# Kernel optimization log

Hardware: AMD Instinct MI355X
Metric: run time of the kernel (lower is better)

Reference implementation:

```python
import jax, jax.numpy as jnp
import numpy as np

N, D, H, E, K = 16384, 1024, 4096, 8, 2
EPS = 1e-5


def setup_inputs() -> dict:
    key = jax.random.key(0)
    ks = jax.random.split(key, 12)
    s = 0.02
    return {
        "x": jax.random.normal(ks[0], (N, D), dtype=jnp.float32),
        "ln_g": jnp.ones((D,), jnp.float32),
        "ln_b": jnp.zeros((D,), jnp.float32),
        "r_w1": jax.random.normal(ks[1], (D, H // 2), jnp.float32) * s,
        "r_b1": jnp.zeros((H // 2,), jnp.float32),
        "r_w2": jax.random.normal(ks[2], (H // 2, E), jnp.float32) * s,
        "r_b2": jnp.zeros((E,), jnp.float32),
        "e_w1": jax.random.normal(ks[3], (E, D, H), jnp.float32) * s,
        "e_b1": jnp.zeros((E, H), jnp.float32),
        "e_w2": jax.random.normal(ks[4], (E, H, D), jnp.float32) * s,
        "e_b2": jnp.zeros((E, D), jnp.float32),
    }


def reference(x, ln_g, ln_b, r_w1, r_b1, r_w2, r_b2, e_w1, e_b1, e_w2, e_b2):
    # LayerNorm
    mu = jnp.mean(x, axis=-1, keepdims=True)
    var = jnp.mean(jnp.square(x - mu), axis=-1, keepdims=True)
    xn = (x - mu) * jax.lax.rsqrt(var + EPS) * ln_g + ln_b  # [N, D]

    # Router: Linear -> ReLU -> Linear -> softmax -> top-k, renormalize
    logits = jax.nn.relu(xn @ r_w1 + r_b1) @ r_w2 + r_b2  # [N, E]
    probs = jax.nn.softmax(logits, axis=-1)
    vals, idx = jax.lax.top_k(probs, K)  # [N, K]
    vals = vals / jnp.sum(vals, axis=-1, keepdims=True)

    # Dense expert dispatch: loop over fixed small E, weight by combine gate
    out = jnp.zeros_like(x)
    for e in range(E):
        gate = jnp.sum(vals * (idx == e).astype(vals.dtype), axis=-1)  # [N]
        h = jax.nn.relu(xn @ e_w1[e] + e_b1[e])  # dropout in eval mode -> identity
        y = h @ e_w2[e] + e_b2[e]  # [N, D]
        out = out + gate[:, None] * y
    return x + out
```

## Files before the change

kernel.cpp:

```cpp
#include <hip/hip_runtime.h>
#include <cstdint>
#include <cstddef>

typedef unsigned short u16;
typedef __attribute__((ext_vector_type(8))) short bf16x8;
typedef __attribute__((ext_vector_type(4))) float f32x4;

#define N_TOK 16384
#define DIM   1024
#define HID   4096
#define NEXP  8
#define HR    2048
#define TAU   0.02f
#define MAXMT 264
#define MAXMT2 136

__device__ __forceinline__ u16 f2bf(float f) {
  union { float f; uint32_t u; } x; x.f = f;
  uint32_t r = x.u + 0x7FFFu + ((x.u >> 16) & 1u);
  return (u16)(r >> 16);
}
__device__ __forceinline__ float bf2f(u16 u) {
  union { uint32_t u; float f; } x; x.u = ((uint32_t)u) << 16; return x.f;
}

__device__ __forceinline__ void async16(const void* g, const void* l) {
  auto gp = reinterpret_cast<const __attribute__((address_space(1))) uint32_t*>(
      reinterpret_cast<uintptr_t>(g));
  auto lp = reinterpret_cast<__attribute__((address_space(3))) uint32_t*>(
      reinterpret_cast<uintptr_t>(l));
  __builtin_amdgcn_global_load_lds(gp, lp, 16, 0, 0);
}

__device__ __forceinline__ unsigned xcd_swz(unsigned flat, unsigned nwg) {
  const unsigned xcd = flat & 7u, lid = flat >> 3;
  const unsigned q = nwg >> 3, r = nwg & 7u;
  return (xcd < r ? xcd * (q + 1u) : r * (q + 1u) + (xcd - r) * q) + lid;
}

template<bool SPLIT>
__global__ __launch_bounds__(256)
void transpose_cvt(const float* __restrict__ src, u16* __restrict__ hi,
                   u16* __restrict__ lo, int R, int C)
{
  __shared__ float tile[64][65];
  const size_t bofs = (size_t)blockIdx.z * R * C;
  src += bofs; hi += bofs; if (SPLIT) lo += bofs;
  const int t = threadIdx.x;
  const int c0 = blockIdx.x * 64, r0 = blockIdx.y * 64;
#pragma unroll
  for (int i = 0; i < 4; ++i) {
    const int idx = i * 256 + t;
    const int rr = idx >> 4;
    const int cc = (idx & 15) << 2;
    const float4 v = *(const float4*)(src + (size_t)(r0 + rr) * C + c0 + cc);
    tile[rr][cc] = v.x; tile[rr][cc + 1] = v.y;
    tile[rr][cc + 2] = v.z; tile[rr][cc + 3] = v.w;
  }
  __syncthreads();
#pragma unroll
  for (int i = 0; i < 4; ++i) {
    const int idx = i * 256 + t;
    const int oc = idx >> 4;
    const int rc = (idx & 15) << 2;
    float v0 = tile[rc][oc], v1 = tile[rc + 1][oc];
    float v2 = tile[rc + 2][oc], v3 = tile[rc + 3][oc];
    ushort4 h;
    h.x = f2bf(v0); h.y = f2bf(v1); h.z = f2bf(v2); h.w = f2bf(v3);
    const size_t o = (size_t)(c0 + oc) * R + r0 + rc;
    *(ushort4*)(hi + o) = h;
    if (SPLIT) {
      ushort4 l;
      l.x = f2bf(v0 - bf2f(h.x)); l.y = f2bf(v1 - bf2f(h.y));
      l.z = f2bf(v2 - bf2f(h.z)); l.w = f2bf(v3 - bf2f(h.w));
      *(ushort4*)(lo + o) = l;
    }
  }
}

__global__ __launch_bounds__(256)
void ln_kernel(const float* __restrict__ x, const float* __restrict__ g,
               const float* __restrict__ b, u16* __restrict__ xh,
               u16* __restrict__ xl, float* __restrict__ out)
{
  const int row = blockIdx.x;
  const int t = threadIdx.x;
  const float4 xv = ((const float4*)(x + (size_t)row * DIM))[t];
  float s = xv.x + xv.y + xv.z + xv.w;
  float q = xv.x * xv.x + xv.y * xv.y + xv.z * xv.z + xv.w * xv.w;
#pragma unroll
  for (int off = 32; off; off >>= 1) {
    s += __shfl_down(s, off, 64);
    q += __shfl_down(q, off, 64);
  }
  __shared__ float sm[8];
  __shared__ float mu_s, rs_s;
  const int lane = t & 63, wv = t >> 6;
  if (lane == 0) { sm[wv] = s; sm[wv + 4] = q; }
  __syncthreads();
  if (t == 0) {
    float S = sm[0] + sm[1] + sm[2] + sm[3];
    float Q = sm[4] + sm[5] + sm[6] + sm[7];
    float mu = S * (1.f / DIM);
    float var = Q * (1.f / DIM) - mu * mu;
    mu_s = mu; rs_s = rsqrtf(var + 1e-5f);
  }
  __syncthreads();
  const float mu = mu_s, rs = rs_s;
  const float4 gv = ((const float4*)g)[t];
  const float4 bv = ((const float4*)b)[t];
  float n0 = (xv.x - mu) * rs * gv.x + bv.x;
  float n1 = (xv.y - mu) * rs * gv.y + bv.y;
  float n2 = (xv.z - mu) * rs * gv.z + bv.z;
  float n3 = (xv.w - mu) * rs * gv.w + bv.w;
  ushort4 h, l;
  h.x = f2bf(n0); l.x = f2bf(n0 - bf2f(h.x));
  h.y = f2bf(n1); l.y = f2bf(n1 - bf2f(h.y));
  h.z = f2bf(n2); l.z = f2bf(n2 - bf2f(h.z));
  h.w = f2bf(n3); l.w = f2bf(n3 - bf2f(h.w));
  ((ushort4*)(xh + (size_t)row * DIM))[t] = h;
  ((ushort4*)(xl + (size_t)row * DIM))[t] = l;
  ((float4*)(out + (size_t)row * DIM))[t] = xv;
}

__global__ __launch_bounds__(256)
void logits_kernel(const u16* __restrict__ HrB, const float* __restrict__ w2,
                   float* __restrict__ logits)
{
  const int row = blockIdx.x, t = threadIdx.x;
  const u16* h = HrB + (size_t)row * HR;
  const ushort4* hv = (const ushort4*)(h + t * 8);
  ushort4 h0 = hv[0], h1 = hv[1];
  u16 hh[8] = {h0.x, h0.y, h0.z, h0.w, h1.x, h1.y, h1.z, h1.w};
  float p[8] = {0, 0, 0, 0, 0, 0, 0, 0};
#pragma unroll
  for (int j = 0; j < 8; ++j) {
    const int col = t * 8 + j;
    const float v = bf2f(hh[j]);
    const float4* wp = (const float4*)(w2 + (size_t)col * 8);
    float4 a = wp[0], b = wp[1];
    p[0] += v * a.x; p[1] += v * a.y; p[2] += v * a.z; p[3] += v * a.w;
    p[4] += v * b.x; p[5] += v * b.y; p[6] += v * b.z; p[7] += v * b.w;
  }
#pragma unroll
  for (int off = 32; off; off >>= 1)
#pragma unroll
    for (int e = 0; e < 8; ++e) p[e] += __shfl_down(p[e], off, 64);
  __shared__ float sm[4][8];
  const int lane = t & 63, wv = t >> 6;
  if (lane == 0) {
#pragma unroll
    for (int e = 0; e < 8; ++e) sm[wv][e] = p[e];
  }
  __syncthreads();
  if (t < 8)
    logits[(size_t)row * 8 + t] = sm[0][t] + sm[1][t] + sm[2][t] + sm[3][t];
}

__device__ __forceinline__ void load_logits(const float* logits, const float* b2,
                                            int row, float l[8]) {
  const float4* lp = (const float4*)(logits + (size_t)row * 8);
  float4 a = lp[0], b = lp[1];
  l[0] = a.x + b2[0]; l[1] = a.y + b2[1]; l[2] = a.z + b2[2]; l[3] = a.w + b2[3];
  l[4] = b.x + b2[4]; l[5] = b.y + b2[5]; l[6] = b.z + b2[6]; l[7] = b.w + b2[7];
}
__device__ __forceinline__ void top2(const float l[8], int& i0, float& l0,
                                     int& i1, float& l1) {
  i0 = 0; l0 = l[0];
#pragma unroll
  for (int e = 1; e < 8; ++e) if (l[e] > l0) { l0 = l[e]; i0 = e; }
  i1 = -1; l1 = -1e30f;
#pragma unroll
  for (int e = 0; e < 8; ++e) if (e != i0 && l[e] > l1) { l1 = l[e]; i1 = e; }
}

__global__ __launch_bounds__(256)
void pass_flag(float* __restrict__ logits, const float* __restrict__ b2,
               int* __restrict__ fixL, int* __restrict__ cntFix)
{
  __shared__ int lcnt;
  __shared__ int base;
  const int t = threadIdx.x;
  const int row = blockIdx.x * 256 + t;
  if (t == 0) lcnt = 0;
  float l[8]; load_logits(logits, b2, row, l);
  int i0, i1; float l0, l1;
  top2(l, i0, l0, i1, l1);
  float l2 = -1e30f;
#pragma unroll
  for (int e = 0; e < 8; ++e)
    if (e != i0 && e != i1 && l[e] > l2) l2 = l[e];
  const bool flag = (l1 - l2) < TAU;
  __syncthreads();
  int r = 0;
  if (flag) r = atomicAdd(&lcnt, 1);
  __syncthreads();
  if (t == 0) base = atomicAdd(cntFix, lcnt);
  __syncthreads();
  if (flag) {
    fixL[base + r] = row;
    float4 z = {0.f, 0.f, 0.f, 0.f};
    ((float4*)(logits + (size_t)row * 8))[0] = z;
    ((float4*)(logits + (size_t)row * 8))[1] = z;
  }
}

__global__ __launch_bounds__(256)
void pass_count(const float* __restrict__ logits, const float* __restrict__ b2,
                int* __restrict__ cnts)
{
  __shared__ int lcnt[NEXP];
  const int t = threadIdx.x;
  const int row = blockIdx.x * 256 + t;
  if (t < NEXP) lcnt[t] = 0;
  float l[8]; load_logits(logits, b2, row, l);
  int i0, i1; float l0, l1;
  top2(l, i0, l0, i1, l1);
  __syncthreads();
  atomicAdd(&lcnt[i0], 1);
  atomicAdd(&lcnt[i1], 1);
  __syncthreads();
  if (t < NEXP) atomicAdd(&cnts[t], lcnt[t]);
}

__global__ void scan_kernel(const int* __restrict__ cnts, int* __restrict__ offs,
                            int* __restrict__ tileOffs, int* __restrict__ tileOffs2)
{
  if (threadIdx.x == 0) {
    int s = 0, ts = 0, ts2 = 0;
#pragma unroll
    for (int e = 0; e < NEXP; ++e) {
      offs[e] = s; s += cnts[e];
      tileOffs[e] = ts; ts += (cnts[e] + 127) >> 7;
      tileOffs2[e] = ts2; ts2 += (cnts[e] + 255) >> 8;
    }
    offs[NEXP] = s;
    tileOffs[NEXP] = ts;
    tileOffs2[NEXP] = ts2;
  }
}

__global__ __launch_bounds__(256)
void pass_scatter(const float* __restrict__ logits, const float* __restrict__ b2,
                  const int* __restrict__ offs, int* __restrict__ cnts2,
                  int* __restrict__ rowsC, float* __restrict__ gateC)
{
  __shared__ int lcnt[NEXP];
  __shared__ int sbase[NEXP];
  const int t = threadIdx.x;
  const int row = blockIdx.x * 256 + t;
  if (t < NEXP) lcnt[t] = 0;
  float l[8]; load_logits(logits, b2, row, l);
  int i0, i1; float l0, l1;
  top2(l, i0, l0, i1, l1);
  float tt = expf(l1 - l0);
  float g0 = 1.f / (1.f + tt);
  float g1 = tt / (1.f + tt);
  __syncthreads();
  int r0 = atomicAdd(&lcnt[i0], 1);
  int r1 = atomicAdd(&lcnt[i1], 1);
  __syncthreads();
  if (t < NEXP) sbase[t] = atomicAdd(&cnts2[t], lcnt[t]);
  __syncthreads();
  int p0 = offs[i0] + sbase[i0] + r0;
  int p1 = offs[i1] + sbase[i1] + r1;
  rowsC[p0] = row; gateC[p0] = g0;
  rowsC[p1] = row; gateC[p1] = g1;
}

#define G8_BAR() do { __builtin_amdgcn_s_barrier(); \
                      __builtin_amdgcn_sched_barrier(0); } while (0)
#define G8_VM4() asm volatile("s_waitcnt vmcnt(4)" ::: "memory")
#define G8_VM0() asm volatile("s_waitcnt vmcnt(0)" ::: "memory")
#define G8_LGKM0() do { asm volatile("s_waitcnt lgkmcnt(0)" ::: "memory"); \
                        __builtin_amdgcn_sched_barrier(0); } while (0)
#define G8_LGKM8() asm volatile("s_waitcnt lgkmcnt(8)" ::: "memory")

#define READ_A(aL, mfh, Af) do { \
  _Pragma("unroll") for (int mf = 0; mf < 4; ++mf) { \
    Af[mf][0] = *(const bf16x8*)&(aL)[((mfh)*4+mf)*1024 + aBase + swzC[0]]; \
    Af[mf][1] = *(const bf16x8*)&(aL)[((mfh)*4+mf)*1024 + aBase + swzC[1]]; \
  } } while (0)

#define READ_B(bL, nfh, Bf) do { \
  _Pragma("unroll") for (int nf = 0; nf < 2; ++nf) { \
    Bf[nf][0] = *(const bf16x8*)&(bL)[((nfh)*2+nf)*1024 + bBase + swzC[0]]; \
    Bf[nf][1] = *(const bf16x8*)&(bL)[((nfh)*2+nf)*1024 + bBase + swzC[1]]; \
  } } while (0)

#define MFMA_Q(mfh, nfh, Af, Bf) do { \
  __builtin_amdgcn_s_setprio(1); \
  _Pragma("unroll") for (int kk = 0; kk < 2; ++kk) \
  _Pragma("unroll") for (int mf = 0; mf < 4; ++mf) \
  _Pragma("unroll") for (int nf = 0; nf < 2; ++nf) \
    acc[(mfh)*4+mf][(nfh)*2+nf] = __builtin_amdgcn_mfma_f32_16x16x32_bf16( \
        Af[mf][kk], Bf[nf][kk], acc[(mfh)*4+mf][(nfh)*2+nf], 0, 0, 0); \
  __builtin_amdgcn_s_setprio(0); } while (0)

template<int EPI, bool GATHER, bool DENSE>
__global__ __launch_bounds__(512, 2)
void gemm8p(const u16* __restrict__ A0, const u16* __restrict__ B0,
            int lda, int ldb, int K, int NT, int ksplit, int Mdense,
            size_t bStrideE, int biasStrideE,
            const int* __restrict__ counts, const int* __restrict__ offs,
            const int* __restrict__ tileOffs,
            const int* __restrict__ rowsC, const float* __restrict__ gatesC,
            const float* __restrict__ bias,
            u16* __restrict__ Cbf, float* __restrict__ Cf32, int ldc)
{
  const unsigned swz = xcd_swz(blockIdx.x, gridDim.x);
  const unsigned ntks = (unsigned)(NT * ksplit);
  const int mt = (int)(swz / ntks);
  int e, m0, Mq, off;
  if constexpr (DENSE) {
    if (mt >= Mdense / 256) return;
    e = 0; m0 = mt * 256; Mq = Mdense; off = 0;
  } else {
    if (mt >= tileOffs[NEXP]) return;
    e = 0;
#pragma unroll
    for (int i = 1; i < NEXP; ++i) if (tileOffs[i] <= mt) e = i;
    m0 = (mt - tileOffs[e]) * 256;
    Mq = counts[e];
    if (m0 >= Mq) return;
    off = offs[e];
  }
  const unsigned rest = swz % ntks;
  const int n0 = (int)(rest / (unsigned)ksplit) * 256;
  const int ks = (int)(rest % (unsigned)ksplit);
  const int Keff = K / ksplit;
  const int kBase = ks * Keff;
  const int* rows = DENSE ? nullptr : (rowsC + off);
  const u16* B = B0 + (size_t)e * bStrideE;
  const float* bi = bias + (size_t)e * biasStrideE;

  __shared__ alignas(16) u16 As[2][2][128 * 64];
  __shared__ alignas(16) u16 Bs[2][2][128 * 64];

  const int t = threadIdx.x;
  const int numK = Keff >> 6;

  const u16* aP[2][2]; const u16* bP[2][2]; int dst[2];
#pragma unroll
  for (int j = 0; j < 2; ++j) {
    const int gdx = j * 512 + t;
    const int rw = gdx >> 3;
    const int cs = (((gdx & 7) ^ (rw & 7)) << 3) + kBase;
    dst[j] = gdx * 8;
#pragma unroll
    for (int h = 0; h < 2; ++h) {
      const int grow = m0 + h * 128 + rw;
      if constexpr (DENSE) {
        aP[h][j] = A0 + (size_t)grow * lda + cs;
      } else {
        const int amc = grow < Mq ? grow : (Mq - 1);
        const size_t agr = GATHER ? (size_t)rows[amc] : (size_t)(off + amc);
        aP[h][j] = A0 + agr * lda + cs;
      }
      bP[h][j] = B + (size_t)(n0 + h * 128 + rw) * ldb + cs;
    }
  }

  auto stA = [&](int tile, int h) {
    async16(aP[h][0] + (size_t)tile * 64, &As[tile & 1][h][dst[0]]);
    async16(aP[h][1] + (size_t)tile * 64, &As[tile & 1][h][dst[1]]);
  };
  auto stB = [&](int tile, int h) {
    async16(bP[h][0] + (size_t)tile * 64, &Bs[tile & 1][h][dst[0]]);
    async16(bP[h][1] + (size_t)tile * 64, &Bs[tile & 1][h][dst[1]]);
  };

  const int lane = t & 63, wv = t >> 6;
  const int wr = wv >> 2;
  const int wc = wv & 3;
  const int fr = lane & 15, fq = lane >> 4;

  int swzC[2];
#pragma unroll
  for (int kk = 0; kk < 2; ++kk)
    swzC[kk] = ((kk * 4 + fq) ^ (fr & 7)) << 3;
  const int aBase = fr * 64;
  const int bBase = (wc & 1) * 4096 + fr * 64;

  const u16* aH[2] = { &As[0][wr][0], &As[1][wr][0] };
  const u16* bH[2] = { &Bs[0][wc >> 1][0], &Bs[1][wc >> 1][0] };

  f32x4 acc[8][4];
#pragma unroll
  for (int i = 0; i < 8; ++i)
#pragma unroll
    for (int j = 0; j < 4; ++j) acc[i][j] = (f32x4){0.f, 0.f, 0.f, 0.f};

  stB(0, 0); stB(0, 1); stA(0, 0); stA(0, 1);
  stB(1, 0); stB(1, 1);
  G8_VM4();
  G8_BAR();

  bf16x8 Af[4][2], Bf0[2][2], Bf1[2][2];

  const int numI = numK >> 1;
  for (int it = 0; it < numI; ++it) {
    const int t1 = 2 * it + 1, t2 = 2 * it + 2, t3 = 2 * it + 3;
    const bool last = (t2 >= numK);
    READ_A(aH[0], 0, Af);
    READ_B(bH[0], 0, Bf0);
    stA(t1, 0);
    G8_LGKM8();
    G8_BAR();
    G8_LGKM0();
    MFMA_Q(0, 0, Af, Bf0);
    G8_BAR();
    READ_B(bH[0], 1, Bf1);
    stA(t1, 1);
    G8_BAR();
    G8_LGKM0();
    MFMA_Q(0, 1, Af, Bf1);
    G8_BAR();
    READ_A(aH[0], 1, Af);
    if (!last) stB(t2, 0);
    G8_BAR();
    G8_LGKM0();
    MFMA_Q(1, 1, Af, Bf1);
    G8_BAR();
    if (!last) stB(t2, 1);
    G8_BAR();
    MFMA_Q(1, 0, Af, Bf0);
    if (last) { G8_VM0(); } else { G8_VM4(); }
    G8_BAR();
    READ_A(aH[1], 0, Af);
    READ_B(bH[1], 0, Bf0);
    if (!last) stA(t2, 0);
    G8_LGKM8();
    G8_BAR();
    G8_LGKM0();
    MFMA_Q(0, 0, Af, Bf0);
    G8_BAR();
    READ_B(bH[1], 1, Bf1);
    if (!last) stA(t2, 1);
    G8_BAR();
    G8_LGKM0();
    MFMA_Q(0, 1, Af, Bf1);
    G8_BAR();
    READ_A(aH[1], 1, Af);
    if (t3 < numK) stB(t3, 0);
    G8_BAR();
    G8_LGKM0();
    MFMA_Q(1, 1, Af, Bf1);
    G8_BAR();
    if (t3 < numK) stB(t3, 1);
    G8_BAR();
    MFMA_Q(1, 0, Af, Bf0);
    if (!last) { G8_VM4(); }
    G8_BAR();
  }

  float bv[4];
#pragma unroll
  for (int nf = 0; nf < 4; ++nf) {
    bv[nf] = bi[n0 + wc * 64 + nf * 16 + fr];
    if (EPI == 2 && ks != 0) bv[nf] = 0.f;
  }

  const int crowBase = DENSE ? 0 : off;
#pragma unroll
  for (int mf = 0; mf < 8; ++mf)
#pragma unroll
    for (int r = 0; r < 4; ++r) {
      const int m = m0 + wr * 128 + mf * 16 + fq * 4 + r;
      if (m < Mq) {
        if constexpr (EPI == 2) {
          const size_t orow = (size_t)rows[m];
          const float g = gatesC[off + m];
#pragma unroll
          for (int nf = 0; nf < 4; ++nf) {
            const int n = n0 + wc * 64 + nf * 16 + fr;
            atomicAdd(&Cf32[orow * ldc + n], g * (acc[mf][nf][r] + bv[nf]));
          }
        } else {
#pragma unroll
          for (int nf = 0; nf < 4; ++nf) {
            const int n = n0 + wc * 64 + nf * 16 + fr;
            Cbf[(size_t)(crowBase + m) * ldc + n] =
                f2bf(fmaxf(acc[mf][nf][r] + bv[nf], 0.f));
          }
        }
      }
    }
}

template<bool SPLIT, int EPI, bool GATHER>
__global__ __launch_bounds__(256, 2)
void gemm_bt(const u16* __restrict__ A0, const u16* __restrict__ A1,
             const u16* __restrict__ B0, const u16* __restrict__ B1,
             int lda, int ldb, int K, int M,
             const int* __restrict__ counts, int expertArg,
             const int* __restrict__ offs,
             const int* __restrict__ rowsC, const float* __restrict__ gatesC,
             const float* __restrict__ bias,
             const float* __restrict__ w2, float* __restrict__ logits,
             u16* __restrict__ Cbf, float* __restrict__ Cf32, int ldc)
{
  int expert, m0, n0;
  if (counts == nullptr) {
    const unsigned nwg = gridDim.x * gridDim.y;
    const unsigned flat = blockIdx.y * gridDim.x + blockIdx.x;
    const unsigned swz = xcd_swz(flat, nwg);
    expert = expertArg;
    m0 = (int)(swz / gridDim.x) * 128;
    n0 = (int)(swz % gridDim.x) * 128;
  } else {
    expert = expertArg;
    m0 = blockIdx.y * 128;
    n0 = blockIdx.x * 128;
  }

  const int Mq = counts ? counts[expert] : M;
  if (m0 >= Mq) return;
  const int off = offs ? offs[expert] : 0;
  const int* rows = rowsC ? rowsC + off : nullptr;
  const float* gates = gatesC ? gatesC + off : nullptr;
  const u16* B = B0;
  const u16* Bl = SPLIT ? B1 : nullptr;
  const float* bi = bias;
  const int z = (int)blockIdx.z;
  const int zOff = z * K;

  __shared__ u16 As0[128 * 32], Bs0[128 * 32];
  __shared__ u16 As1[SPLIT ? 128 * 32 : 8], Bs1[SPLIT ? 128 * 32 : 8];

  const int t = threadIdx.x;
  size_t aoff[2]; int acodd[2]; size_t boff[2];
#pragma unroll
  for (int i = 0; i < 2; ++i) {
    int gdx = i * 256 + t;
    int ar = gdx >> 2, ac = (gdx & 3) * 8;
    int am = m0 + ar;
    int amc = am < Mq ? am : (Mq - 1);
    int agr = GATHER ? rows[amc] : amc;
    aoff[i] = (size_t)agr * lda + ac + zOff;
    boff[i] = (size_t)(n0 + ar) * ldb + ac + zOff;
    acodd[i] = gdx * 8;
  }

  f32x4 acc[4][4];
#pragma unroll
  for (int i = 0; i < 4; ++i)
#pragma unroll
    for (int j = 0; j < 4; ++j) acc[i][j] = (f32x4){0.f, 0.f, 0.f, 0.f};

  const int lane = t & 63, wv = t >> 6;
  const int wm = (wv >> 1) * 64, wn = (wv & 1) * 64;
  const int fr = lane & 15, fq = lane >> 4;

  for (int k0 = 0; k0 < K; k0 += 32) {
    __syncthreads();
#pragma unroll
    for (int i = 0; i < 2; ++i) {
      async16(A0 + aoff[i] + k0, &As0[acodd[i]]);
      async16(B + boff[i] + k0, &Bs0[acodd[i]]);
      if (SPLIT) {
        async16(A1 + aoff[i] + k0, &As1[acodd[i]]);
        async16(Bl + boff[i] + k0, &Bs1[acodd[i]]);
      }
    }
    __syncthreads();
    bf16x8 af[4], bfr[4], af1[4], bf1[4];
#pragma unroll
    for (int xi = 0; xi < 4; ++xi) {
      af[xi]  = *(const bf16x8*)&As0[(wm + xi * 16 + fr) * 32 + fq * 8];
      bfr[xi] = *(const bf16x8*)&Bs0[(wn + xi * 16 + fr) * 32 + fq * 8];
      if (SPLIT) {
        af1[xi] = *(const bf16x8*)&As1[(wm + xi * 16 + fr) * 32 + fq * 8];
        bf1[xi] = *(const bf16x8*)&Bs1[(wn + xi * 16 + fr) * 32 + fq * 8];
      }
    }
#pragma unroll
    for (int mt = 0; mt < 4; ++mt)
#pragma unroll
      for (int nt = 0; nt < 4; ++nt) {
        acc[mt][nt] = __builtin_amdgcn_mfma_f32_16x16x32_bf16(af[mt], bfr[nt], acc[mt][nt], 0, 0, 0);
        if (SPLIT) {
          acc[mt][nt] = __builtin_amdgcn_mfma_f32_16x16x32_bf16(af[mt], bf1[nt], acc[mt][nt], 0, 0, 0);
          acc[mt][nt] = __builtin_amdgcn_mfma_f32_16x16x32_bf16(af1[mt], bfr[nt], acc[mt][nt], 0, 0, 0);
        }
      }
  }

  if constexpr (EPI == 3) {
    float w2v[4][8]; float b1v[4];
#pragma unroll
    for (int nt = 0; nt < 4; ++nt) {
      const int n = n0 + wn + nt * 16 + fr;
      b1v[nt] = bi[n];
      const float4* wp = (const float4*)(w2 + (size_t)n * 8);
      float4 wa = wp[0], wb = wp[1];
      w2v[nt][0] = wa.x; w2v[nt][1] = wa.y; w2v[nt][2] = wa.z; w2v[nt][3] = wa.w;
      w2v[nt][4] = wb.x; w2v[nt][5] = wb.y; w2v[nt][6] = wb.z; w2v[nt][7] = wb.w;
    }
#pragma unroll
    for (int mt = 0; mt < 4; ++mt) {
      float pe[4][8];
#pragma unroll
      for (int r = 0; r < 4; ++r)
#pragma unroll
        for (int ee = 0; ee < 8; ++ee) pe[r][ee] = 0.f;
#pragma unroll
      for (int nt = 0; nt < 4; ++nt)
#pragma unroll
        for (int r = 0; r < 4; ++r) {
          float v = fmaxf(acc[mt][nt][r] + b1v[nt], 0.f);
#pragma unroll
          for (int ee = 0; ee < 8; ++ee) pe[r][ee] += v * w2v[nt][ee];
        }
#pragma unroll
      for (int offx = 1; offx < 16; offx <<= 1)
#pragma unroll
        for (int r = 0; r < 4; ++r)
#pragma unroll
          for (int ee = 0; ee < 8; ++ee)
            pe[r][ee] += __shfl_xor(pe[r][ee], offx, 64);
      if (fr == 0) {
#pragma unroll
        for (int r = 0; r < 4; ++r) {
          const int m = m0 + wm + mt * 16 + fq * 4 + r;
          if (m < Mq) {
            const int lrow = GATHER ? rows[m] : m;
#pragma unroll
            for (int ee = 0; ee < 8; ++ee)
              atomicAdd(&logits[(size_t)lrow * 8 + ee], pe[r][ee]);
          }
        }
      }
    }
    return;
  }

#pragma unroll
  for (int mt = 0; mt < 4; ++mt) {
#pragma unroll
    for (int nt = 0; nt < 4; ++nt) {
      const int n = n0 + wn + nt * 16 + fr;
      const float bvv = (z == 0) ? bi[n] : 0.f;
#pragma unroll
      for (int r = 0; r < 4; ++r) {
        const int m = m0 + wm + mt * 16 + fq * 4 + r;
        if (m < Mq) {
          float v = acc[mt][nt][r] + bvv;
          if constexpr (EPI == 1) {
            Cbf[(size_t)m * ldc + n] = f2bf(fmaxf(v, 0.f));
          } else {
            atomicAdd(&Cf32[(size_t)rows[m] * ldc + n], gates[m] * v);
          }
        }
      }
    }
  }
}

extern "C" void kernel_launch(void* const* d_in, const int* in_sizes, int n_in,
                              void* d_out, int out_size, void* d_ws, size_t ws_size,
                              hipStream_t stream)
{
  const float* x    = (const float*)d_in[0];
  const float* ln_g = (const float*)d_in[1];
  const float* ln_b = (const float*)d_in[2];
  const float* r_w1 = (const float*)d_in[3];
  const float* r_b1 = (const float*)d_in[4];
  const float* r_w2 = (const float*)d_in[5];
  const float* r_b2 = (const float*)d_in[6];
  const float* e_w1 = (const float*)d_in[7];
  const float* e_b1 = (const float*)d_in[8];
  const float* e_w2 = (const float*)d_in[9];
  const float* e_b2 = (const float*)d_in[10];
  float* out = (float*)d_out;

  char* ws = (char*)d_ws;
  const size_t MB = 1024ull * 1024ull;
  u16*   xnhi = (u16*)(ws);
  u16*   xnlo = (u16*)(ws + 32 * MB);
  u16*   rw1h = (u16*)(ws + 64 * MB);
  u16*   rw1l = (u16*)(ws + 68 * MB);
  u16*   ew1t = (u16*)(ws + 72 * MB);
  u16*   ew2t = (u16*)(ws + 136 * MB);
  float* logits = (float*)(ws + 200 * MB);
  int*   rowsC  = (int*)(ws + 200 * MB + 512 * 1024);
  float* gateC  = (float*)(ws + 200 * MB + 640 * 1024);
  int*   fixL   = (int*)(ws + 200 * MB + 768 * 1024);
  int*   cntb   = (int*)(ws + 200 * MB + 832 * 1024);
  int*   cnts   = cntb;
  int*   cnts2  = cntb + 8;
  int*   offs   = cntb + 16;
  int*   cntFix = cntb + 25;
  int*   tileOffs  = cntb + 32;
  int*   tileOffs2 = cntb + 48;
  u16*   Hbuf = (u16*)(ws + 201 * MB);
  u16*   HrB  = Hbuf;
  (void)in_sizes; (void)n_in; (void)out_size;

  const bool fused = ws_size >= 458ull * MB;

  hipMemsetAsync(cntb, 0, 256, stream);

  transpose_cvt<true ><<<dim3(HR / 64, DIM / 64, 1), 256, 0, stream>>>(r_w1, rw1h, rw1l, DIM, HR);
  transpose_cvt<false><<<dim3(HID / 64, DIM / 64, NEXP), 256, 0, stream>>>(e_w1, ew1t, nullptr, DIM, HID);
  transpose_cvt<false><<<dim3(DIM / 64, HID / 64, NEXP), 256, 0, stream>>>(e_w2, ew2t, nullptr, HID, DIM);

  ln_kernel<<<N_TOK, 256, 0, stream>>>(x, ln_g, ln_b, xnhi, xnlo, out);

  gemm8p<1, false, true><<<dim3((HR / 256) * (N_TOK / 256)), 512, 0, stream>>>(
      xnhi, rw1h, DIM, DIM, DIM, HR / 256, 1, N_TOK, 0, 0,
      nullptr, nullptr, nullptr, nullptr, nullptr, r_b1,
      HrB, nullptr, HR);

  logits_kernel<<<N_TOK, 256, 0, stream>>>(HrB, r_w2, logits);

  pass_flag<<<N_TOK / 256, 256, 0, stream>>>(logits, r_b2, fixL, cntFix);

  gemm_bt<true, 3, true><<<dim3(HR / 128, N_TOK / 128), 256, 0, stream>>>(
      xnhi, xnlo, rw1h, rw1l, DIM, DIM, DIM, N_TOK,
      cntFix, 0, nullptr, fixL, nullptr, r_b1, r_w2, logits,
      nullptr, nullptr, 0);

  pass_count<<<N_TOK / 256, 256, 0, stream>>>(logits, r_b2, cnts);
  scan_kernel<<<1, 64, 0, stream>>>(cnts, offs, tileOffs, tileOffs2);
  pass_scatter<<<N_TOK / 256, 256, 0, stream>>>(logits, r_b2, offs, cnts2, rowsC, gateC);

  if (fused) {
    gemm8p<1, true, false><<<dim3((HID / 256) * MAXMT2), 512, 0, stream>>>(
        xnhi, ew1t, DIM, DIM, DIM, HID / 256, 1, 0,
        (size_t)HID * DIM, HID,
        cnts, offs, tileOffs2, rowsC, nullptr, e_b1,
        Hbuf, nullptr, HID);
    gemm8p<2, false, false><<<dim3((DIM / 256) * MAXMT2), 512, 0, stream>>>(
        Hbuf, ew2t, HID, HID, HID, DIM / 256, 1, 0,
        (size_t)DIM * HID, DIM,
        cnts, offs, tileOffs2, rowsC, gateC, e_b2,
        nullptr, out, DIM);
  } else {
    for (int e = 0; e < NEXP; ++e) {
      gemm_bt<false, 1, true><<<dim3(HID / 128, N_TOK / 128), 256, 0, stream>>>(
          xnhi, nullptr, ew1t + (size_t)e * HID * DIM, nullptr,
          DIM, DIM, DIM, N_TOK,
          cnts, e, offs, rowsC, nullptr, e_b1 + (size_t)e * HID, nullptr, nullptr,
          Hbuf, nullptr, HID);
      gemm_bt<false, 2, false><<<dim3(DIM / 128, N_TOK / 128, 2), 256, 0, stream>>>(
          Hbuf, nullptr, ew2t + (size_t)e * DIM * HID, nullptr,
          HID, HID, HID / 2, N_TOK,
          cnts, e, offs, rowsC, gateC, e_b2 + (size_t)e * DIM, nullptr, nullptr,
          nullptr, out, DIM);
    }
  }
}
```

Measured before the change: 1.386 ms.

## Fuse expert up and down GEMMs into persistent kernel with work queue

Replaces the two separate grouped expert GEMM launches with one persistent kernel of 256 workgroups. Each workgroup pulls tiles from an atomic work counter: up-projection tiles first, then down-projection tiles. Down-projection tiles spin-wait on per-row-tile ready counters that up-projection tiles bump after writing their output. This overlaps the tail of the first GEMM with the start of the second and removes a launch boundary, at the cost of spin-wait stalls, one workgroup per CU, and dependence on queue ordering for forward progress. The dense router GEMM kernel is also trimmed to a dense-only template.

```diff
diff --git a/kernel.cpp b/kernel.cpp
--- a/kernel.cpp
+++ b/kernel.cpp
@@ -297,70 +297,102 @@
         Af[mf][kk], Bf[nf][kk], acc[(mfh)*4+mf][(nfh)*2+nf], 0, 0, 0); \
   __builtin_amdgcn_s_setprio(0); } while (0)
 
-template<int EPI, bool GATHER, bool DENSE>
+#define G8_KLOOP() do { \
+  stB(0, 0); stB(0, 1); stA(0, 0); stA(0, 1); \
+  stB(1, 0); stB(1, 1); \
+  G8_VM4(); \
+  G8_BAR(); \
+  bf16x8 Af[4][2], Bf0[2][2], Bf1[2][2]; \
+  const int numI = numK >> 1; \
+  for (int it = 0; it < numI; ++it) { \
+    const int t1 = 2 * it + 1, t2 = 2 * it + 2, t3 = 2 * it + 3; \
+    const bool last = (t2 >= numK); \
+    READ_A(aH[0], 0, Af); \
+    READ_B(bH[0], 0, Bf0); \
+    stA(t1, 0); \
+    G8_LGKM8(); \
+    G8_BAR(); \
+    G8_LGKM0(); \
+    MFMA_Q(0, 0, Af, Bf0); \
+    G8_BAR(); \
+    READ_B(bH[0], 1, Bf1); \
+    stA(t1, 1); \
+    G8_BAR(); \
+    G8_LGKM0(); \
+    MFMA_Q(0, 1, Af, Bf1); \
+    G8_BAR(); \
+    READ_A(aH[0], 1, Af); \
+    if (!last) stB(t2, 0); \
+    G8_BAR(); \
+    G8_LGKM0(); \
+    MFMA_Q(1, 1, Af, Bf1); \
+    G8_BAR(); \
+    if (!last) stB(t2, 1); \
+    G8_BAR(); \
+    MFMA_Q(1, 0, Af, Bf0); \
+    if (last) { G8_VM0(); } else { G8_VM4(); } \
+    G8_BAR(); \
+    READ_A(aH[1], 0, Af); \
+    READ_B(bH[1], 0, Bf0); \
+    if (!last) stA(t2, 0); \
+    G8_LGKM8(); \
+    G8_BAR(); \
+    G8_LGKM0(); \
+    MFMA_Q(0, 0, Af, Bf0); \
+    G8_BAR(); \
+    READ_B(bH[1], 1, Bf1); \
+    if (!last) stA(t2, 1); \
+    G8_BAR(); \
+    G8_LGKM0(); \
+    MFMA_Q(0, 1, Af, Bf1); \
+    G8_BAR(); \
+    READ_A(aH[1], 1, Af); \
+    if (t3 < numK) stB(t3, 0); \
+    G8_BAR(); \
+    G8_LGKM0(); \
+    MFMA_Q(1, 1, Af, Bf1); \
+    G8_BAR(); \
+    if (t3 < numK) stB(t3, 1); \
+    G8_BAR(); \
+    MFMA_Q(1, 0, Af, Bf0); \
+    if (!last) { G8_VM4(); } \
+    G8_BAR(); \
+  } \
+} while (0)
+
+template<int EPI>
 __global__ __launch_bounds__(512, 2)
 void gemm8p(const u16* __restrict__ A0, const u16* __restrict__ B0,
-            int lda, int ldb, int K, int NT, int ksplit, int Mdense,
-            size_t bStrideE, int biasStrideE,
-            const int* __restrict__ counts, const int* __restrict__ offs,
-            const int* __restrict__ tileOffs,
-            const int* __restrict__ rowsC, const float* __restrict__ gatesC,
+            int lda, int ldb, int K, int NT, int Mdense,
             const float* __restrict__ bias,
-            u16* __restrict__ Cbf, float* __restrict__ Cf32, int ldc)
+            u16* __restrict__ Cbf, int ldc)
 {
   const unsigned swz = xcd_swz(blockIdx.x, gridDim.x);
-  const unsigned ntks = (unsigned)(NT * ksplit);
-  const int mt = (int)(swz / ntks);
-  int e, m0, Mq, off;
-  if constexpr (DENSE) {
-    if (mt >= Mdense / 256) return;
-    e = 0; m0 = mt * 256; Mq = Mdense; off = 0;
-  } else {
-    if (mt >= tileOffs[NEXP]) return;
-    e = 0;
-#pragma unroll
-    for (int i = 1; i < NEXP; ++i) if (tileOffs[i] <= mt) e = i;
-    m0 = (mt - tileOffs[e]) * 256;
-    Mq = counts[e];
-    if (m0 >= Mq) return;
-    off = offs[e];
-  }
-  const unsigned rest = swz % ntks;
-  const int n0 = (int)(rest / (unsigned)ksplit) * 256;
-  const int ks = (int)(rest % (unsigned)ksplit);
-  const int Keff = K / ksplit;
-  const int kBase = ks * Keff;
-  const int* rows = DENSE ? nullptr : (rowsC + off);
-  const u16* B = B0 + (size_t)e * bStrideE;
-  const float* bi = bias + (size_t)e * biasStrideE;
+  const int mt = (int)(swz / (unsigned)NT);
+  if (mt >= Mdense / 256) return;
+  const int m0 = mt * 256, Mq = Mdense;
+  const int n0 = (int)(swz % (unsigned)NT) * 256;
+  const float* bi = bias;
 
   __shared__ alignas(16) u16 As[2][2][128 * 64];
   __shared__ alignas(16) u16 Bs[2][2][128 * 64];
 
   const int t = threadIdx.x;
-  const int numK = Keff >> 6;
+  const int numK = K >> 6;
 
   const u16* aP[2][2]; const u16* bP[2][2]; int dst[2];
 #pragma unroll
   for (int j = 0; j < 2; ++j) {
     const int gdx = j * 512 + t;
     const int rw = gdx >> 3;
-    const int cs = (((gdx & 7) ^ (rw & 7)) << 3) + kBase;
+    const int cs = ((gdx & 7) ^ (rw & 7)) << 3;
     dst[j] = gdx * 8;
 #pragma unroll
     for (int h = 0; h < 2; ++h) {
-      const int grow = m0 + h * 128 + rw;
-      if constexpr (DENSE) {
-        aP[h][j] = A0 + (size_t)grow * lda + cs;
-      } else {
-        const int amc = grow < Mq ? grow : (Mq - 1);
-        const size_t agr = GATHER ? (size_t)rows[amc] : (size_t)(off + amc);
-        aP[h][j] = A0 + agr * lda + cs;
-      }
-      bP[h][j] = B + (size_t)(n0 + h * 128 + rw) * ldb + cs;
-    }
-  }
-
+      aP[h][j] = A0 + (size_t)(m0 + h * 128 + rw) * lda + cs;
+      bP[h][j] = B0 + (size_t)(n0 + h * 128 + rw) * ldb + cs;
+    }
+  }
   auto stA = [&](int tile, int h) {
     async16(aP[h][0] + (size_t)tile * 64, &As[tile & 1][h][dst[0]]);
     async16(aP[h][1] + (size_t)tile * 64, &As[tile & 1][h][dst[1]]);
@@ -371,17 +403,14 @@
   };
 
   const int lane = t & 63, wv = t >> 6;
-  const int wr = wv >> 2;
-  const int wc = wv & 3;
+  const int wr = wv >> 2, wc = wv & 3;
   const int fr = lane & 15, fq = lane >> 4;
-
   int swzC[2];
 #pragma unroll
   for (int kk = 0; kk < 2; ++kk)
     swzC[kk] = ((kk * 4 + fq) ^ (fr & 7)) << 3;
   const int aBase = fr * 64;
   const int bBase = (wc & 1) * 4096 + fr * 64;
-
   const u16* aH[2] = { &As[0][wr][0], &As[1][wr][0] };
   const u16* bH[2] = { &Bs[0][wc >> 1][0], &Bs[1][wc >> 1][0] };
 
@@ -391,101 +420,172 @@
 #pragma unroll
     for (int j = 0; j < 4; ++j) acc[i][j] = (f32x4){0.f, 0.f, 0.f, 0.f};
 
-  stB(0, 0); stB(0, 1); stA(0, 0); stA(0, 1);
-  stB(1, 0); stB(1, 1);
-  G8_VM4();
-  G8_BAR();
-
-  bf16x8 Af[4][2], Bf0[2][2], Bf1[2][2];
-
-  const int numI = numK >> 1;
-  for (int it = 0; it < numI; ++it) {
-    const int t1 = 2 * it + 1, t2 = 2 * it + 2, t3 = 2 * it + 3;
-    const bool last = (t2 >= numK);
-    READ_A(aH[0], 0, Af);
-    READ_B(bH[0], 0, Bf0);
-    stA(t1, 0);
-    G8_LGKM8();
-    G8_BAR();
-    G8_LGKM0();
-    MFMA_Q(0, 0, Af, Bf0);
-    G8_BAR();
-    READ_B(bH[0], 1, Bf1);
-    stA(t1, 1);
-    G8_BAR();
-    G8_LGKM0();
-    MFMA_Q(0, 1, Af, Bf1);
-    G8_BAR();
-    READ_A(aH[0], 1, Af);
-    if (!last) stB(t2, 0);
-    G8_BAR();
-    G8_LGKM0();
-    MFMA_Q(1, 1, Af, Bf1);
-    G8_BAR();
-    if (!last) stB(t2, 1);
-    G8_BAR();
-    MFMA_Q(1, 0, Af, Bf0);
-    if (last) { G8_VM0(); } else { G8_VM4(); }
-    G8_BAR();
-    READ_A(aH[1], 0, Af);
-    READ_B(bH[1], 0, Bf0);
-    if (!last) stA(t2, 0);
-    G8_LGKM8();
-    G8_BAR();
-    G8_LGKM0();
-    MFMA_Q(0, 0, Af, Bf0);
-    G8_BAR();
-    READ_B(bH[1], 1, Bf1);
-    if (!last) stA(t2, 1);
-    G8_BAR();
-    G8_LGKM0();
-    MFMA_Q(0, 1, Af, Bf1);
-    G8_BAR();
-    READ_A(aH[1], 1, Af);
-    if (t3 < numK) stB(t3, 0);
-    G8_BAR();
-    G8_LGKM0();
-    MFMA_Q(1, 1, Af, Bf1);
-    G8_BAR();
-    if (t3 < numK) stB(t3, 1);
-    G8_BAR();
-    MFMA_Q(1, 0, Af, Bf0);
-    if (!last) { G8_VM4(); }
-    G8_BAR();
-  }
+  G8_KLOOP();
 
   float bv[4];
 #pragma unroll
-  for (int nf = 0; nf < 4; ++nf) {
-    bv[nf] = bi[n0 + wc * 64 + nf * 16 + fr];
-    if (EPI == 2 && ks != 0) bv[nf] = 0.f;
-  }
-
-  const int crowBase = DENSE ? 0 : off;
+  for (int nf = 0; nf < 4; ++nf) bv[nf] = bi[n0 + wc * 64 + nf * 16 + fr];
 #pragma unroll
   for (int mf = 0; mf < 8; ++mf)
 #pragma unroll
     for (int r = 0; r < 4; ++r) {
       const int m = m0 + wr * 128 + mf * 16 + fq * 4 + r;
       if (m < Mq) {
-        if constexpr (EPI == 2) {
-          const size_t orow = (size_t)rows[m];
-          const float g = gatesC[off + m];
-#pragma unroll
-          for (int nf = 0; nf < 4; ++nf) {
-            const int n = n0 + wc * 64 + nf * 16 + fr;
-            atomicAdd(&Cf32[orow * ldc + n], g * (acc[mf][nf][r] + bv[nf]));
-          }
-        } else {
-#pragma unroll
-          for (int nf = 0; nf < 4; ++nf) {
-            const int n = n0 + wc * 64 + nf * 16 + fr;
-            Cbf[(size_t)(crowBase + m) * ldc + n] =
-                f2bf(fmaxf(acc[mf][nf][r] + bv[nf], 0.f));
+#pragma unroll
+        for (int nf = 0; nf < 4; ++nf) {
+          const int n = n0 + wc * 64 + nf * 16 + fr;
+          Cbf[(size_t)m * ldc + n] = f2bf(fmaxf(acc[mf][nf][r] + bv[nf], 0.f));
+        }
+      }
+    }
+}
+
+__global__ __launch_bounds__(512, 1)
+void moe_fused(const u16* __restrict__ xnhi, const u16* __restrict__ ew1t,
+               const u16* __restrict__ ew2t,
+               const int* __restrict__ counts, const int* __restrict__ offs,
+               const int* __restrict__ tileOffs2,
+               const int* __restrict__ rowsC, const float* __restrict__ gatesC,
+               const float* __restrict__ e_b1, const float* __restrict__ e_b2,
+               u16* __restrict__ Hbuf, float* __restrict__ out,
+               int* __restrict__ qctr, int* __restrict__ ready)
+{
+  constexpr int NT1 = HID / 256;
+  constexpr int NT2 = DIM / 256;
+  constexpr int W1 = NT1 * MAXMT2;
+  constexpr int WTOT = W1 + NT2 * MAXMT2;
+
+  __shared__ alignas(16) u16 As[2][2][128 * 64];
+  __shared__ alignas(16) u16 Bs[2][2][128 * 64];
+  __shared__ int sh_w;
+
+  const int t = threadIdx.x;
+  const int lane = t & 63, wv = t >> 6;
+  const int wr = wv >> 2, wc = wv & 3;
+  const int fr = lane & 15, fq = lane >> 4;
+  int swzC[2];
+#pragma unroll
+  for (int kk = 0; kk < 2; ++kk)
+    swzC[kk] = ((kk * 4 + fq) ^ (fr & 7)) << 3;
+  const int aBase = fr * 64;
+  const int bBase = (wc & 1) * 4096 + fr * 64;
+  const u16* aH[2] = { &As[0][wr][0], &As[1][wr][0] };
+  const u16* bH[2] = { &Bs[0][wc >> 1][0], &Bs[1][wc >> 1][0] };
+
+  for (;;) {
+    __syncthreads();
+    if (t == 0) sh_w = atomicAdd(qctr, 1);
+    __syncthreads();
+    const int w = sh_w;
+    if (w >= WTOT) return;
+    const bool isG1 = (w < W1);
+    const int wl = isG1 ? w : (w - W1);
+    const int NT = isG1 ? NT1 : NT2;
+    const int mt = wl / NT;
+    if (mt >= tileOffs2[NEXP]) continue;
+    int e = 0;
+#pragma unroll
+    for (int i = 1; i < NEXP; ++i) if (tileOffs2[i] <= mt) e = i;
+    const int m0 = (mt - tileOffs2[e]) * 256;
+    const int Mq = counts[e];
+    if (m0 >= Mq) continue;
+    const int off = offs[e];
+    const int n0 = (wl % NT) * 256;
+
+    if (!isG1) {
+      if (t == 0) {
+        while (__hip_atomic_load(ready + mt, __ATOMIC_ACQUIRE,
+                                 __HIP_MEMORY_SCOPE_AGENT) < NT1)
+          __builtin_amdgcn_s_sleep(8);
+      }
+      __syncthreads();
+    }
+
+    const int lda = isG1 ? DIM : HID;
+    const int numK = (isG1 ? DIM : HID) >> 6;
+    const u16* Asrc = isG1 ? xnhi : Hbuf;
+    const u16* B = isG1 ? (ew1t + (size_t)e * HID * DIM)
+                        : (ew2t + (size_t)e * DIM * HID);
+    const float* bi = isG1 ? (e_b1 + (size_t)e * HID)
+                           : (e_b2 + (size_t)e * DIM);
+    const int* rows = rowsC + off;
+
+    const u16* aP[2][2]; const u16* bP[2][2]; int dst[2];
+#pragma unroll
+    for (int j = 0; j < 2; ++j) {
+      const int gdx = j * 512 + t;
+      const int rw = gdx >> 3;
+      const int cs = ((gdx & 7) ^ (rw & 7)) << 3;
+      dst[j] = gdx * 8;
+#pragma unroll
+      for (int h = 0; h < 2; ++h) {
+        const int grow = m0 + h * 128 + rw;
+        const int amc = grow < Mq ? grow : (Mq - 1);
+        const size_t agr = isG1 ? (size_t)rows[amc] : (size_t)(off + amc);
+        aP[h][j] = Asrc + agr * lda + cs;
+        bP[h][j] = B + (size_t)(n0 + h * 128 + rw) * lda + cs;
+      }
+    }
+    auto stA = [&](int tile, int h) {
+      async16(aP[h][0] + (size_t)tile * 64, &As[tile & 1][h][dst[0]]);
+      async16(aP[h][1] + (size_t)tile * 64, &As[tile & 1][h][dst[1]]);
+    };
+    auto stB = [&](int tile, int h) {
+      async16(bP[h][0] + (size_t)tile * 64, &Bs[tile & 1][h][dst[0]]);
+      async16(bP[h][1] + (size_t)tile * 64, &Bs[tile & 1][h][dst[1]]);
+    };
+
+    f32x4 acc[8][4];
+#pragma unroll
+    for (int i = 0; i < 8; ++i)
+#pragma unroll
+      for (int j = 0; j < 4; ++j) acc[i][j] = (f32x4){0.f, 0.f, 0.f, 0.f};
+
+    asm volatile("s_waitcnt vmcnt(0)" ::: "memory");
+
+    G8_KLOOP();
+
+    float bv[4];
+#pragma unroll
+    for (int nf = 0; nf < 4; ++nf) bv[nf] = bi[n0 + wc * 64 + nf * 16 + fr];
+
+    if (isG1) {
+#pragma unroll
+      for (int mf = 0; mf < 8; ++mf)
+#pragma unroll
+        for (int r = 0; r < 4; ++r) {
+          const int m = m0 + wr * 128 + mf * 16 + fq * 4 + r;
+          if (m < Mq) {
+#pragma unroll
+            for (int nf = 0; nf < 4; ++nf) {
+              const int n = n0 + wc * 64 + nf * 16 + fr;
+              Hbuf[(size_t)(off + m) * HID + n] =
+                  f2bf(fmaxf(acc[mf][nf][r] + bv[nf], 0.f));
+            }
           }
         }
-      }
-    }
+      __syncthreads();
+      if (t == 0)
+        __hip_atomic_fetch_add(ready + mt, 1, __ATOMIC_RELEASE,
+                               __HIP_MEMORY_SCOPE_AGENT);
+    } else {
+#pragma unroll
+      for (int mf = 0; mf < 8; ++mf)
+#pragma unroll
+        for (int r = 0; r < 4; ++r) {
+          const int m = m0 + wr * 128 + mf * 16 + fq * 4 + r;
+          if (m < Mq) {
+            const size_t orow = (size_t)rows[m];
+            const float g = gatesC[off + m];
+#pragma unroll
+            for (int nf = 0; nf < 4; ++nf) {
+              const int n = n0 + wc * 64 + nf * 16 + fr;
+              atomicAdd(&out[orow * DIM + n], g * (acc[mf][nf][r] + bv[nf]));
+            }
+          }
+        }
+    }
+  }
 }
 
 template<bool SPLIT, int EPI, bool GATHER>
@@ -693,6 +793,9 @@
   int*   cntFix = cntb + 25;
   int*   tileOffs  = cntb + 32;
   int*   tileOffs2 = cntb + 48;
+  int*   qready = (int*)(ws + 200 * MB + 836 * 1024);
+  int*   qctr   = qready;
+  int*   ready  = qready + 16;
   u16*   Hbuf = (u16*)(ws + 201 * MB);
   u16*   HrB  = Hbuf;
   (void)in_sizes; (void)n_in; (void)out_size;
@@ -700,6 +803,7 @@
   const bool fused = ws_size >= 458ull * MB;
 
   hipMemsetAsync(cntb, 0, 256, stream);
+  hipMemsetAsync(qready, 0, 4096, stream);
 
   transpose_cvt<true ><<<dim3(HR / 64, DIM / 64, 1), 256, 0, stream>>>(r_w1, rw1h, rw1l, DIM, HR);
   transpose_cvt<false><<<dim3(HID / 64, DIM / 64, NEXP), 256, 0, stream>>>(e_w1, ew1t, nullptr, DIM, HID);
@@ -707,10 +811,8 @@
 
   ln_kernel<<<N_TOK, 256, 0, stream>>>(x, ln_g, ln_b, xnhi, xnlo, out);
 
-  gemm8p<1, false, true><<<dim3((HR / 256) * (N_TOK / 256)), 512, 0, stream>>>(
-      xnhi, rw1h, DIM, DIM, DIM, HR / 256, 1, N_TOK, 0, 0,
-      nullptr, nullptr, nullptr, nullptr, nullptr, r_b1,
-      HrB, nullptr, HR);
+  gemm8p<1><<<dim3((HR / 256) * (N_TOK / 256)), 512, 0, stream>>>(
+      xnhi, rw1h, DIM, DIM, DIM, HR / 256, N_TOK, r_b1, HrB, HR);
 
   logits_kernel<<<N_TOK, 256, 0, stream>>>(HrB, r_w2, logits);
 
@@ -726,16 +828,9 @@
   pass_scatter<<<N_TOK / 256, 256, 0, stream>>>(logits, r_b2, offs, cnts2, rowsC, gateC);
 
   if (fused) {
-    gemm8p<1, true, false><<<dim3((HID / 256) * MAXMT2), 512, 0, stream>>>(
-        xnhi, ew1t, DIM, DIM, DIM, HID / 256, 1, 0,
-        (size_t)HID * DIM, HID,
-        cnts, offs, tileOffs2, rowsC, nullptr, e_b1,
-        Hbuf, nullptr, HID);
-    gemm8p<2, false, false><<<dim3((DIM / 256) * MAXMT2), 512, 0, stream>>>(
-        Hbuf, ew2t, HID, HID, HID, DIM / 256, 1, 0,
-        (size_t)DIM * HID, DIM,
-        cnts, offs, tileOffs2, rowsC, gateC, e_b2,
-        nullptr, out, DIM);
+    moe_fused<<<dim3(256), 512, 0, stream>>>(
+        xnhi, ew1t, ew2t, cnts, offs, tileOffs2, rowsC, gateC,
+        e_b1, e_b2, Hbuf, out, qctr, ready);
   } else {
     for (int e = 0; e < NEXP; ++e) {
       gemm_bt<false, 1, true><<<dim3(HID / 128, N_TOK / 128), 256, 0, stream>>>(
```

After: 1.397 ms. About the same (+0.8%).
